# Optimization experiments

Measured on AMD Instinct MI355X. Metric: run time of the kernel, lower is better.

Reference implementation:

```python
import jax, jax.numpy as jnp
import numpy as np

H, C = 4, 32          # GAT heads, per-head dim
NH = 4                # transformer heads


def layer_norm(x, g, b, eps=1e-5):
    mu = x.mean(-1, keepdims=True)
    var = ((x - mu) ** 2).mean(-1, keepdims=True)
    return (x - mu) / jnp.sqrt(var + eps) * g + b


def setup_inputs() -> dict:
    key = jax.random.key(0)
    ks = jax.random.split(key, 16)
    B, T, N, F = 256, 72, 5, 10
    D, FF = 128, 256
    # full directed graph on 5 stations, no self loops (E=20)
    ei = np.array([[i, j] for i in range(N) for j in range(N) if i != j], dtype=np.int32).T
    s = 0.1
    return {
        'x': jax.random.normal(ks[0], (B, T, N, F), jnp.float32),
        'edge_index': jnp.asarray(ei),
        'gcn_w': jax.random.normal(ks[1], (F, 64), jnp.float32) * s,
        'gcn_b': jnp.zeros((64,), jnp.float32),
        'gat_w': jax.random.normal(ks[2], (64, H * C), jnp.float32) * s,
        'gat_a_src': jax.random.normal(ks[3], (H, C), jnp.float32) * s,
        'gat_a_dst': jax.random.normal(ks[4], (H, C), jnp.float32) * s,
        'gat_b': jnp.zeros((H * C,), jnp.float32),
        'gln_g': jnp.ones((D,), jnp.float32),
        'gln_b': jnp.zeros((D,), jnp.float32),
        'tw_qkv': jax.random.normal(ks[5], (3, D, 3 * D), jnp.float32) * s,
        'tb_qkv': jnp.zeros((3, 3 * D), jnp.float32),
        'tw_o': jax.random.normal(ks[6], (3, D, D), jnp.float32) * s,
        'tb_o': jnp.zeros((3, D), jnp.float32),
        'ln1_g': jnp.ones((3, D), jnp.float32),
        'ln1_b': jnp.zeros((3, D), jnp.float32),
        'w_ff1': jax.random.normal(ks[7], (3, D, FF), jnp.float32) * s,
        'b_ff1': jnp.zeros((3, FF), jnp.float32),
        'w_ff2': jax.random.normal(ks[8], (3, FF, D), jnp.float32) * s,
        'b_ff2': jnp.zeros((3, D), jnp.float32),
        'ln2_g': jnp.ones((3, D), jnp.float32),
        'ln2_b': jnp.zeros((3, D), jnp.float32),
        'hw1': jax.random.normal(ks[9], (6, D, D // 2), jnp.float32) * s,
        'hb1': jnp.zeros((6, D // 2), jnp.float32),
        'hw2': jax.random.normal(ks[10], (6, D // 2, 5), jnp.float32) * s,
        'hb2': jnp.zeros((6, 5), jnp.float32),
    }


def reference(x, edge_index, gcn_w, gcn_b, gat_w, gat_a_src, gat_a_dst, gat_b,
              gln_g, gln_b, tw_qkv, tb_qkv, tw_o, tb_o, ln1_g, ln1_b,
              w_ff1, b_ff1, w_ff2, b_ff2, ln2_g, ln2_b, hw1, hb1, hw2, hb2):
    B, T, N, F = x.shape
    D = gln_g.shape[0]

    # ---- frozen GCN encoder (torch.no_grad): symmetric-normalized A with self loops
    src, dst = edge_index[0], edge_index[1]
    loop = jnp.arange(N, dtype=src.dtype)
    src2 = jnp.concatenate([src, loop])
    dst2 = jnp.concatenate([dst, loop])
    A = jnp.zeros((N, N), x.dtype).at[dst2, src2].add(1.0)
    deg = A.sum(1)
    dinv = jnp.where(deg > 0, deg ** -0.5, 0.0)
    Anorm = dinv[:, None] * A * dinv[None, :]
    xw = jnp.einsum('btnf,fh->btnh', x, gcn_w) + gcn_b
    gcn = jnp.tanh(jnp.einsum('ij,btjh->btih', Anorm, xw))
    gcn = jax.lax.stop_gradient(gcn)  # encoder is frozen + no_grad

    # ---- GATConv over batched graph (self loops added, PyG default), eval mode (no dropout)
    h = jnp.einsum('btnf,fhc->btnhc', gcn, gat_w.reshape(gcn.shape[-1], H, C))
    a_s = (h * gat_a_src).sum(-1)                         # [B,T,N,H]
    a_d = (h * gat_a_dst).sum(-1)
    e = a_s[:, :, src2, :] + a_d[:, :, dst2, :]           # [B,T,E2,H]
    e = jnp.where(e > 0, e, 0.2 * e)                      # LeakyReLU(0.2)
    eT = jnp.moveaxis(e, 2, 0)                            # [E2,B,T,H]
    m = jax.ops.segment_max(eT, dst2, num_segments=N)
    ex = jnp.exp(eT - m[dst2])
    denom = jax.ops.segment_sum(ex, dst2, num_segments=N)
    alpha = ex / denom[dst2]                              # scatter-softmax per dst node
    hsrc = jnp.moveaxis(h, 2, 0)[src2]                    # [E2,B,T,H,C]
    agg = jax.ops.segment_sum(alpha[..., None] * hsrc, dst2, num_segments=N)
    gat = jnp.moveaxis(agg, 0, 2).reshape(B, T, N, H * C) + gat_b
    gat = layer_norm(gat, gln_g, gln_b)

    # ---- mean-pool stations, positional encoding
    z = gat.mean(2)                                       # [B,T,D]
    pos = jnp.arange(T, dtype=jnp.float32)[:, None]
    div = jnp.exp(jnp.arange(0, D, 2, dtype=jnp.float32) * (-np.log(10000.0) / D))
    pe = jnp.zeros((T, D), x.dtype).at[:, 0::2].set(jnp.sin(pos * div)).at[:, 1::2].set(jnp.cos(pos * div))
    z = z + pe

    # ---- post-norm transformer encoder (relu FF), eval mode
    dh = D // NH
    scale = jnp.sqrt(jnp.asarray(dh, x.dtype))
    for i in range(tw_qkv.shape[0]):
        qkv = z @ tw_qkv[i] + tb_qkv[i]
        q, k, v = jnp.split(qkv, 3, axis=-1)
        q = q.reshape(B, T, NH, dh)
        k = k.reshape(B, T, NH, dh)
        v = v.reshape(B, T, NH, dh)
        att = jax.nn.softmax(jnp.einsum('bqhd,bkhd->bhqk', q, k) / scale, axis=-1)
        o = jnp.einsum('bhqk,bkhd->bqhd', att, v).reshape(B, T, D)
        z = layer_norm(z + o @ tw_o[i] + tb_o[i], ln1_g[i], ln1_b[i])
        ff = jax.nn.relu(z @ w_ff1[i] + b_ff1[i]) @ w_ff2[i] + b_ff2[i]
        z = layer_norm(z + ff, ln2_g[i], ln2_b[i])

    # ---- multi-horizon forecast heads on last timestep -> stacked [6,B,5]
    last = z[:, -1]
    h1 = jax.nn.relu(jnp.einsum('bd,kdm->kbm', last, hw1) + hb1[:, None, :])
    out = jnp.einsum('kbm,kms->kbs', h1, hw2) + hb2[:, None, :]
    return out
```

## Files before the change

### kernel.cpp

```cpp
#include <hip/hip_runtime.h>
#include <hip/hip_bf16.h>

#define B_  256
#define T_  72
#define N_  5
#define F_  10
#define D_  128
#define HH_ 4
#define CC_ 32
#define FF_ 256
#define BT_ (B_*T_)
#define E2MAX 32

#define WS_Z    256
#define WS_QKV  (WS_Z + BT_*D_)
#define WS_OBUF (WS_QKV + BT_*3*D_)
#define WS_WBF  (WS_OBUF + BT_*D_)

#define WOFF_QKV(i)  ((i)*49152)
#define WOFF_O(i)    (147456 + (i)*16384)
#define WOFF_FF1(i)  (196608 + (i)*32768)
#define WOFF_FF2(i)  (294912 + (i)*32768)
#define WOFF_GATW    393216

#define MZF_OFF   0
#define MSB_OFF   38016
#define MSQ_OFF   70784
#define MSK_OFF   92544
#define MVT_OFF   114304
#define MOB_OFF   140928
#define MSMEM_BYTES 162688

typedef __attribute__((ext_vector_type(8))) short bf16x8;
typedef __attribute__((ext_vector_type(4))) float f32x4;

__device__ __forceinline__ unsigned short bf16_rne(float x) {
    unsigned u = __float_as_uint(x);
    unsigned r = (u + 0x7FFFu + ((u >> 16) & 1u)) >> 16;
    return (unsigned short)r;
}
__device__ __forceinline__ unsigned bf16pk(float a, float b) {
    return (unsigned)bf16_rne(a) | ((unsigned)bf16_rne(b) << 16);
}
__device__ __forceinline__ float bf2f(short s) {
    return __uint_as_float(((unsigned)(unsigned short)s) << 16);
}
__device__ __forceinline__ bf16x8 cvt8(const float* p) {
    float4 a = *(const float4*)p;
    float4 b = *(const float4*)(p + 4);
    unsigned u[4] = {bf16pk(a.x, a.y), bf16pk(a.z, a.w), bf16pk(b.x, b.y), bf16pk(b.z, b.w)};
    return *(bf16x8*)u;
}

__global__ void setup_kernel(const int* __restrict__ ei, float* __restrict__ ws, int E) {
    if (threadIdx.x != 0 || blockIdx.x != 0) return;
    int* wsi = (int*)ws;
    const int N = N_;
    int E2 = E + N;
    int src2[E2MAX], dst2[E2MAX];
    for (int e = 0; e < E; ++e) { src2[e] = ei[e]; dst2[e] = ei[E + e]; }
    for (int n = 0; n < N; ++n) { src2[E + n] = n; dst2[E + n] = n; }
    float A[N_ * N_];
    for (int i = 0; i < N * N; ++i) A[i] = 0.f;
    for (int e = 0; e < E2; ++e) A[dst2[e] * N + src2[e]] += 1.f;
    float dinv[N_];
    for (int n = 0; n < N; ++n) {
        float s = 0.f;
        for (int j = 0; j < N; ++j) s += A[n * N + j];
        dinv[n] = (s > 0.f) ? rsqrtf(s) : 0.f;
    }
    for (int n = 0; n < N; ++n)
        for (int j = 0; j < N; ++j)
            ws[n * N + j] = dinv[n] * A[n * N + j] * dinv[j];
    int cnt[N_];
    for (int n = 0; n < N; ++n) cnt[n] = 0;
    for (int e = 0; e < E2; ++e) cnt[dst2[e]]++;
    int off = 0;
    for (int n = 0; n < N; ++n) { wsi[96 + n] = off; off += cnt[n]; }
    wsi[96 + N] = off;
    int cur[N_];
    for (int n = 0; n < N; ++n) cur[n] = wsi[96 + n];
    for (int e = 0; e < E2; ++e) wsi[104 + cur[dst2[e]]++] = e;
    for (int e = 0; e < E2; ++e) { wsi[32 + e] = src2[e]; wsi[64 + e] = dst2[e]; }
}

__global__ __launch_bounds__(256) void prep_kernel(
    const float* __restrict__ tw_qkv, const float* __restrict__ tw_o,
    const float* __restrict__ w_ff1, const float* __restrict__ w_ff2,
    const float* __restrict__ gat_w, short* __restrict__ wbf)
{
    __shared__ float s_t[64][65];
    const int tid = threadIdx.x;
    int t = blockIdx.x;
    const float* src; short* dst; int R, C, tr, tc;
    if (t >= 96) { int q = t - 96; src = gat_w; dst = wbf + WOFF_GATW; R = 64; C = 128; tr = 0; tc = q; }
    else {
        int layer = t / 32, r32 = t % 32;
        if (r32 < 12)      { src = tw_qkv + layer * (128*384); dst = wbf + WOFF_QKV(layer); R = 128; C = 384; tr = r32 / 6;  tc = r32 % 6; }
        else if (r32 < 16) { int q = r32 - 12; src = tw_o + layer * 16384; dst = wbf + WOFF_O(layer);  R = 128; C = 128; tr = q >> 1; tc = q & 1; }
        else if (r32 < 24) { int q = r32 - 16; src = w_ff1 + layer * 32768; dst = wbf + WOFF_FF1(layer); R = 128; C = 256; tr = q >> 2; tc = q & 3; }
        else               { int q = r32 - 24; src = w_ff2 + layer * 32768; dst = wbf + WOFF_FF2(layer); R = 256; C = 128; tr = q >> 1; tc = q & 1; }
    }
    #pragma unroll
    for (int it = 0; it < 16; ++it) {
        int e = it * 256 + tid;
        int r = e >> 6, c = e & 63;
        s_t[r][c] = src[(size_t)(tr*64 + r) * C + tc*64 + c];
    }
    __syncthreads();
    #pragma unroll
    for (int it = 0; it < 16; ++it) {
        int e = it * 256 + tid;
        int c = e >> 6, r = e & 63;
        dst[(size_t)(tc*64 + c) * R + tr*64 + r] = (short)bf16_rne(s_t[r][c]);
    }
}

__device__ __forceinline__ bf16x8 ld_frag(const short* s, int row, int kbase, int ldk) {
    return *(const bf16x8*)&s[row * ldk + (kbase ^ ((row & 7) << 3))];
}
__device__ __forceinline__ void stage_b(short* s_b, const short* __restrict__ src, int tid) {
    const uint4* s4 = (const uint4*)src;
    #pragma unroll
    for (int it = 0; it < 8; ++it) {
        int c = it * 256 + tid;
        int row = c >> 4, ke = (c & 15) * 8;
        *(uint4*)&s_b[row * 128 + (ke ^ ((row & 7) << 3))] = s4[c];
    }
}

__global__ __launch_bounds__(256) void gcn_h_mfma(
    const float* __restrict__ x, const float* __restrict__ gcn_w, const float* __restrict__ gcn_b,
    const float* __restrict__ a_src, const float* __restrict__ a_dst,
    const float* __restrict__ ws, const short* __restrict__ gwT,
    short* __restrict__ hbuf, float* __restrict__ asb, float* __restrict__ adb)
{
    __shared__ float s_x[16 * 50];
    __shared__ float s_an[25];
    __shared__ short s_gcn[80 * 64];

    const int tid = threadIdx.x;
    const int tok0 = blockIdx.x * 16;

    for (int i = tid; i < 16 * 50; i += 256) s_x[i] = x[(size_t)tok0 * 50 + i];
    if (tid < 25) s_an[tid] = ws[tid];
    __syncthreads();

    #pragma unroll
    for (int it = 0; it < 2; ++it) {
        int idx = it * 256 + tid;
        int tl = idx >> 5, kp = idx & 31;
        int k0 = kp * 2;
        float w0[F_], w1[F_];
        #pragma unroll
        for (int f = 0; f < F_; ++f) { w0[f] = gcn_w[f * 64 + k0]; w1[f] = gcn_w[f * 64 + k0 + 1]; }
        float b0 = gcn_b[k0], b1 = gcn_b[k0 + 1];
        float xw0[N_], xw1[N_];
        #pragma unroll
        for (int n = 0; n < N_; ++n) {
            float a0 = b0, a1 = b1;
            #pragma unroll
            for (int f = 0; f < F_; ++f) {
                float xv = s_x[tl * 50 + n * 10 + f];
                a0 += xv * w0[f]; a1 += xv * w1[f];
            }
            xw0[n] = a0; xw1[n] = a1;
        }
        #pragma unroll
        for (int n = 0; n < N_; ++n) {
            float s0 = 0.f, s1 = 0.f;
            #pragma unroll
            for (int j = 0; j < N_; ++j) { float an = s_an[n * 5 + j]; s0 += an * xw0[j]; s1 += an * xw1[j]; }
            float e0 = __expf(2.f * fabsf(s0)), e1 = __expf(2.f * fabsf(s1));
            float t0 = copysignf(1.f - 2.f / (e0 + 1.f), s0);
            float t1 = copysignf(1.f - 2.f / (e1 + 1.f), s1);
            int row = tl * 5 + n;
            *(unsigned*)&s_gcn[row * 64 + (k0 ^ ((row & 7) << 3))] = bf16pk(t0, t1);
        }
    }
    __syncthreads();

    const int w = tid >> 6, lane = tid & 63;
    const int c = lane & 15, g = lane >> 4;
    const int kf = g * 8;
    bf16x8 bfr[2][2];
    #pragma unroll
    for (int nn = 0; nn < 2; ++nn)
        #pragma unroll
        for (int k0 = 0; k0 < 2; ++k0)
            bfr[nn][k0] = *(const bf16x8*)&gwT[(w * 32 + nn * 16 + c) * 64 + k0 * 32 + kf];
    const float as0 = a_src[w * 32 + c],      as1 = a_src[w * 32 + 16 + c];
    const float ad0 = a_dst[w * 32 + c],      ad1 = a_dst[w * 32 + 16 + c];
    #pragma unroll
    for (int m = 0; m < 5; ++m) {
        bf16x8 af0 = ld_frag(s_gcn, m * 16 + c, kf, 64);
        bf16x8 af1 = ld_frag(s_gcn, m * 16 + c, 32 + kf, 64);
        f32x4 a0 = {0,0,0,0}, a1 = {0,0,0,0};
        a0 = __builtin_amdgcn_mfma_f32_16x16x32_bf16(af0, bfr[0][0], a0, 0, 0, 0);
        a0 = __builtin_amdgcn_mfma_f32_16x16x32_bf16(af1, bfr[0][1], a0, 0, 0, 0);
        a1 = __builtin_amdgcn_mfma_f32_16x16x32_bf16(af0, bfr[1][0], a1, 0, 0, 0);
        a1 = __builtin_amdgcn_mfma_f32_16x16x32_bf16(af1, bfr[1][1], a1, 0, 0, 0);
        float ps[4], pd[4];
        #pragma unroll
        for (int i = 0; i < 4; ++i) {
            int row = m * 16 + g * 4 + i;
            size_t gr = (size_t)(tok0 * 5 + row) * 128;
            hbuf[gr + w * 32 + c]      = (short)bf16_rne(a0[i]);
            hbuf[gr + w * 32 + 16 + c] = (short)bf16_rne(a1[i]);
            ps[i] = a0[i] * as0 + a1[i] * as1;
            pd[i] = a0[i] * ad0 + a1[i] * ad1;
        }
        #pragma unroll
        for (int mm = 1; mm < 16; mm <<= 1)
            #pragma unroll
            for (int i = 0; i < 4; ++i) { ps[i] += __shfl_xor(ps[i], mm); pd[i] += __shfl_xor(pd[i], mm); }
        if (c == 0) {
            #pragma unroll
            for (int i = 0; i < 4; ++i) {
                int row = m * 16 + g * 4 + i;
                asb[(size_t)(tok0 * 5 + row) * 4 + w] = ps[i];
                adb[(size_t)(tok0 * 5 + row) * 4 + w] = pd[i];
            }
        }
    }
}

__global__ __launch_bounds__(256) void gat_agg(
    const short* __restrict__ hbuf, const float* __restrict__ asb, const float* __restrict__ adb,
    const float* __restrict__ gat_b, const float* __restrict__ gln_g, const float* __restrict__ gln_b,
    const float* __restrict__ ws, float* __restrict__ z, int E2)
{
    __shared__ int   s_src[E2MAX], s_csr_off[N_ + 1], s_csr_e[E2MAX];
    __shared__ float s_alpha[4][E2MAX][4];
    __shared__ short s_h[4 * 5 * 128];

    const int tid = threadIdx.x;
    const int wv = tid >> 6, lane = tid & 63;
    const int tok = blockIdx.x * 4 + wv;
    const int* wsi = (const int*)ws;

    if (tid < E2) { s_src[tid] = wsi[32 + tid]; s_csr_e[tid] = wsi[104 + tid]; }
    if (tid < N_ + 1) s_csr_off[tid] = wsi[96 + tid];
    {
        const uint4* hb4 = (const uint4*)(hbuf + (size_t)blockIdx.x * 4 * 5 * 128);
        uint4* sh4 = (uint4*)s_h;
        #pragma unroll
        for (int it = 0; it < 2; ++it) {
            int i = it * 256 + tid;
            if (i < 320) sh4[i] = hb4[i];
        }
    }
    __syncthreads();

    if (lane < 20) {
        int dn = lane >> 2, head = lane & 3;
        int j0 = s_csr_off[dn], j1 = s_csr_off[dn + 1];
        float adv = adb[(size_t)(tok * 5 + dn) * 4 + head];
        float mx = -1e30f;
        for (int j = j0; j < j1; ++j) {
            int e = s_csr_e[j];
            float ev = asb[(size_t)(tok * 5 + s_src[e]) * 4 + head] + adv;
            ev = ev > 0.f ? ev : 0.2f * ev;
            mx = fmaxf(mx, ev);
        }
        float den = 0.f;
        for (int j = j0; j < j1; ++j) {
            int e = s_csr_e[j];
            float ev = asb[(size_t)(tok * 5 + s_src[e]) * 4 + head] + adv;
            ev = ev > 0.f ? ev : 0.2f * ev;
            float ex = __expf(ev - mx);
            den += ex;
            s_alpha[wv][e][head] = ex;
        }
        float r = 1.f / den;
        for (int j = j0; j < j1; ++j) s_alpha[wv][s_csr_e[j]][head] *= r;
    }
    __syncthreads();

    const int h0 = lane >> 5, h1 = 2 + (lane >> 5);
    const float gb0 = gat_b[lane],      gb1 = gat_b[lane + 64];
    const float gg0 = gln_g[lane],      gg1 = gln_g[lane + 64];
    const float gB0 = gln_b[lane],      gB1 = gln_b[lane + 64];
    float v0[N_], v1[N_];
    #pragma unroll
    for (int n = 0; n < N_; ++n) {
        float a0 = 0.f, a1 = 0.f;
        int j0 = s_csr_off[n], j1 = s_csr_off[n + 1];
        for (int j = j0; j < j1; ++j) {
            int e = s_csr_e[j];
            int rb = (wv * 5 + s_src[e]) * 128;
            a0 += s_alpha[wv][e][h0] * bf2f(s_h[rb + lane]);
            a1 += s_alpha[wv][e][h1] * bf2f(s_h[rb + lane + 64]);
        }
        v0[n] = a0 + gb0; v1[n] = a1 + gb1;
    }
    float r1[N_], r2[N_];
    #pragma unroll
    for (int n = 0; n < N_; ++n) { r1[n] = v0[n] + v1[n]; r2[n] = v0[n]*v0[n] + v1[n]*v1[n]; }
    #pragma unroll
    for (int mm = 1; mm < 64; mm <<= 1)
        #pragma unroll
        for (int n = 0; n < N_; ++n) { r1[n] += __shfl_xor(r1[n], mm); r2[n] += __shfl_xor(r2[n], mm); }
    float z0 = 0.f, z1 = 0.f;
    #pragma unroll
    for (int n = 0; n < N_; ++n) {
        float mu = r1[n] * (1.f / D_);
        float var = r2[n] * (1.f / D_) - mu * mu;
        float rstd = rsqrtf(var + 1e-5f);
        z0 += (v0[n] - mu) * rstd * gg0 + gB0;
        z1 += (v1[n] - mu) * rstd * gg1 + gB1;
    }
    z0 *= (1.f / N_); z1 *= (1.f / N_);
    const float cpe = -9.210340371976184f / (float)D_;
    int t = tok % T_;
    float dv0 = __expf((float)(lane & ~1) * cpe);
    float dv1 = __expf((float)((lane + 64) & ~1) * cpe);
    float ang0 = (float)t * dv0, ang1 = (float)t * dv1;
    z0 += (lane & 1) ? __cosf(ang0) : __sinf(ang0);
    z1 += (lane & 1) ? __cosf(ang1) : __sinf(ang1);
    z[(size_t)tok * D_ + lane] = z0;
    z[(size_t)tok * D_ + 64 + lane] = z1;
}

__global__ __launch_bounds__(256, 1) void layers_fused(
    const float* __restrict__ zg, const short* __restrict__ wbf,
    const float* __restrict__ tb_qkv, const float* __restrict__ tb_o,
    const float* __restrict__ ln1_g, const float* __restrict__ ln1_b,
    const float* __restrict__ b_ff1, const float* __restrict__ b_ff2,
    const float* __restrict__ ln2_g, const float* __restrict__ ln2_b,
    const float* __restrict__ hw1, const float* __restrict__ hb1,
    const float* __restrict__ hw2, const float* __restrict__ hb2,
    float* __restrict__ out)
{
    extern __shared__ char smem[];
    float* s_zf = (float*)(smem + MZF_OFF);
    short* s_b  = (short*)(smem + MSB_OFF);
    short* s_q  = (short*)(smem + MSQ_OFF);
    short* s_k  = (short*)(smem + MSK_OFF);
    short* s_vt = (short*)(smem + MVT_OFF);
    short* s_ob = (short*)(smem + MOB_OFF);
    short* s_f  = s_q;
    short* s_z1 = s_vt;

    const int tid = threadIdx.x;
    const int w = tid >> 6, lane = tid & 63;
    const int c = lane & 15, g = lane >> 4;
    const int kf = g * 8;
    const int b = blockIdx.x;

    for (int idx = tid; idx < 72 * 128; idx += 256) {
        int r = idx >> 7, col = idx & 127;
        s_zf[r * 132 + col] = zg[(size_t)(b * T_ + r) * D_ + col];
    }
    for (int idx = tid; idx < 128 * 32; idx += 256) {
        int ch = idx >> 5, key = 72 + (idx & 31);
        s_vt[ch * 104 + key] = 0;
    }
    __syncthreads();

    for (int L = 0; L < 3; ++L) {
        const short* Wq = wbf + WOFF_QKV(L);
        const short* Wo = wbf + WOFF_O(L);
        const short* W1 = wbf + WOFF_FF1(L);
        const short* W2 = wbf + WOFF_FF2(L);
        const float* bq = tb_qkv + L * 384;
        const float* bo = tb_o + L * D_;
        const float* g1 = ln1_g + L * D_, *be1 = ln1_b + L * D_;
        const float* b1 = b_ff1 + L * FF_, *b2 = b_ff2 + L * D_;
        const float* g2 = ln2_g + L * D_, *be2 = ln2_b + L * D_;

        for (int ch = 0; ch < 3; ++ch) {
            __syncthreads();
            stage_b(s_b, Wq + ch * 16384, tid);
            __syncthreads();
            bf16x8 Bf[2][4];
            float bvj[2];
            #pragma unroll
            for (int j = 0; j < 2; ++j) {
                int n0 = w * 2 + j;
                int brow = n0 * 16 + c;
                #pragma unroll
                for (int k0 = 0; k0 < 4; ++k0) Bf[j][k0] = ld_frag(s_b, brow, k0 * 32 + kf, 128);
                bvj[j] = bq[ch * 128 + n0 * 16 + c];
            }
            #pragma unroll
            for (int m = 0; m < 5; ++m) {
                int arow = m * 16 + c;
                bool valid = arow < 72;
                bf16x8 Af[4];
                bf16x8 z8 = {0,0,0,0,0,0,0,0};
                #pragma unroll
                for (int k0 = 0; k0 < 4; ++k0)
                    Af[k0] = valid ? cvt8(&s_zf[arow * 132 + k0 * 32 + kf]) : z8;
                #pragma unroll
                for (int j = 0; j < 2; ++j) {
                    int n0 = w * 2 + j;
                    f32x4 acc = {bvj[j], bvj[j], bvj[j], bvj[j]};
                    #pragma unroll
                    for (int k0 = 0; k0 < 4; ++k0)
                        acc = __builtin_amdgcn_mfma_f32_16x16x32_bf16(Af[k0], Bf[j][k0], acc, 0, 0, 0);
                    int wcol = n0 * 16 + c;
                    #pragma unroll
                    for (int i = 0; i < 4; ++i) {
                        int lrow = m * 16 + g * 4 + i;
                        short v = (short)bf16_rne(acc[i]);
                        if (ch == 0)      s_q[lrow * 136 + wcol] = v;
                        else if (ch == 1) s_k[lrow * 136 + wcol] = v;
                        else              s_vt[wcol * 104 + lrow] = v;
                    }
                }
            }
        }
        __syncthreads();

        {
            short* pstrip = s_b + w * 16 * 104;
            for (int t2 = lane; t2 < 16 * 16; t2 += 64) {
                int r = t2 >> 4, col = 80 + (t2 & 15);
                pstrip[r * 104 + col] = 0;
            }
            const float scale = 0.17677669529663687f;
            #pragma unroll
            for (int m = 0; m < 5; ++m) {
                bf16x8 aq = *(const bf16x8*)&s_q[(m * 16 + c) * 136 + w * 32 + kf];
                float ps[5][4], mx[4], den[4];
                #pragma unroll
                for (int i = 0; i < 4; ++i) mx[i] = -1e30f;
                #pragma unroll
                for (int n0 = 0; n0 < 5; ++n0) {
                    bf16x8 bk = *(const bf16x8*)&s_k[(n0 * 16 + c) * 136 + w * 32 + kf];
                    f32x4 z4 = {0,0,0,0};
                    f32x4 accS = __builtin_amdgcn_mfma_f32_16x16x32_bf16(aq, bk, z4, 0, 0, 0);
                    #pragma unroll
                    for (int i = 0; i < 4; ++i) {
                        float s = accS[i] * scale;
                        if (n0 == 4 && c >= 8) s = -1e30f;
                        ps[n0][i] = s;
                        mx[i] = fmaxf(mx[i], s);
                    }
                }
                #pragma unroll
                for (int mm = 1; mm < 16; mm <<= 1)
                    #pragma unroll
                    for (int i = 0; i < 4; ++i) mx[i] = fmaxf(mx[i], __shfl_xor(mx[i], mm));
                #pragma unroll
                for (int i = 0; i < 4; ++i) den[i] = 0.f;
                #pragma unroll
                for (int n0 = 0; n0 < 5; ++n0)
                    #pragma unroll
                    for (int i = 0; i < 4; ++i) { float e = __expf(ps[n0][i] - mx[i]); ps[n0][i] = e; den[i] += e; }
                #pragma unroll
                for (int mm = 1; mm < 16; mm <<= 1)
                    #pragma unroll
                    for (int i = 0; i < 4; ++i) den[i] += __shfl_xor(den[i], mm);
                float rden[4];
                #pragma unroll
                for (int i = 0; i < 4; ++i) rden[i] = 1.f / den[i];
                #pragma unroll
                for (int n0 = 0; n0 < 5; ++n0)
                    #pragma unroll
                    for (int i = 0; i < 4; ++i)
                        pstrip[(g * 4 + i) * 104 + n0 * 16 + c] = (short)bf16_rne(ps[n0][i] * rden[i]);
                f32x4 accO[2] = {{0,0,0,0},{0,0,0,0}};
                #pragma unroll
                for (int kt = 0; kt < 3; ++kt) {
                    bf16x8 ap = *(const bf16x8*)&pstrip[c * 104 + kt * 32 + kf];
                    #pragma unroll
                    for (int n0 = 0; n0 < 2; ++n0) {
                        bf16x8 bv = *(const bf16x8*)&s_vt[(w * 32 + n0 * 16 + c) * 104 + kt * 32 + kf];
                        accO[n0] = __builtin_amdgcn_mfma_f32_16x16x32_bf16(ap, bv, accO[n0], 0, 0, 0);
                    }
                }
                #pragma unroll
                for (int n0 = 0; n0 < 2; ++n0)
                    #pragma unroll
                    for (int i = 0; i < 4; ++i)
                        s_ob[(m * 16 + g * 4 + i) * 136 + w * 32 + n0 * 16 + c] = (short)bf16_rne(accO[n0][i]);
            }
        }
        __syncthreads();

        stage_b(s_b, Wo, tid);
        __syncthreads();
        for (int m = w; m < 5; m += 4) {
            bf16x8 Af[4];
            #pragma unroll
            for (int k0 = 0; k0 < 4; ++k0)
                Af[k0] = *(const bf16x8*)&s_ob[(m * 16 + c) * 136 + k0 * 32 + kf];
            f32x4 acc[8];
            #pragma unroll
            for (int n0 = 0; n0 < 8; ++n0) {
                float bv = bo[n0 * 16 + c];
                acc[n0] = (f32x4){bv, bv, bv, bv};
                int brow = n0 * 16 + c;
                #pragma unroll
                for (int k0 = 0; k0 < 4; ++k0) {
                    bf16x8 bfg = ld_frag(s_b, brow, k0 * 32 + kf, 128);
                    acc[n0] = __builtin_amdgcn_mfma_f32_16x16x32_bf16(Af[k0], bfg, acc[n0], 0, 0, 0);
                }
            }
            #pragma unroll
            for (int n0 = 0; n0 < 8; ++n0)
                #pragma unroll
                for (int i = 0; i < 4; ++i) {
                    int row = m * 16 + g * 4 + i;
                    acc[n0][i] += (row < 72) ? s_zf[row * 132 + n0 * 16 + c] : 0.f;
                }
            float s1[4] = {0,0,0,0}, s2[4] = {0,0,0,0};
            #pragma unroll
            for (int n0 = 0; n0 < 8; ++n0)
                #pragma unroll
                for (int i = 0; i < 4; ++i) { float v = acc[n0][i]; s1[i] += v; s2[i] += v * v; }
            #pragma unroll
            for (int mm = 1; mm < 16; mm <<= 1)
                #pragma unroll
                for (int i = 0; i < 4; ++i) { s1[i] += __shfl_xor(s1[i], mm); s2[i] += __shfl_xor(s2[i], mm); }
            #pragma unroll
            for (int i = 0; i < 4; ++i) {
                float mu = s1[i] * (1.f / D_);
                float var = s2[i] * (1.f / D_) - mu * mu;
                float rstd = rsqrtf(var + 1e-5f);
                int row = m * 16 + g * 4 + i;
                #pragma unroll
                for (int n0 = 0; n0 < 8; ++n0) {
                    float v = (acc[n0][i] - mu) * rstd * g1[n0 * 16 + c] + be1[n0 * 16 + c];
                    if (row < 72) s_zf[row * 132 + n0 * 16 + c] = v;
                    s_z1[row * 136 + n0 * 16 + c] = (short)bf16_rne(v);
                }
            }
        }

        for (int ch = 0; ch < 2; ++ch) {
            __syncthreads();
            stage_b(s_b, W1 + ch * 16384, tid);
            __syncthreads();
            bf16x8 Bf[2][4];
            float bvj[2];
            #pragma unroll
            for (int j = 0; j < 2; ++j) {
                int n0 = w * 2 + j;
                int brow = n0 * 16 + c;
                #pragma unroll
                for (int k0 = 0; k0 < 4; ++k0) Bf[j][k0] = ld_frag(s_b, brow, k0 * 32 + kf, 128);
                bvj[j] = b1[ch * 128 + n0 * 16 + c];
            }
            #pragma unroll
            for (int m = 0; m < 5; ++m) {
                bf16x8 Af[4];
                #pragma unroll
                for (int k0 = 0; k0 < 4; ++k0)
                    Af[k0] = *(const bf16x8*)&s_z1[(m * 16 + c) * 136 + k0 * 32 + kf];
                #pragma unroll
                for (int j = 0; j < 2; ++j) {
                    int n0 = w * 2 + j;
                    f32x4 acc = {bvj[j], bvj[j], bvj[j], bvj[j]};
                    #pragma unroll
                    for (int k0 = 0; k0 < 4; ++k0)
                        acc = __builtin_amdgcn_mfma_f32_16x16x32_bf16(Af[k0], Bf[j][k0], acc, 0, 0, 0);
                    #pragma unroll
                    for (int i = 0; i < 4; ++i) {
                        int lrow = m * 16 + g * 4 + i;
                        s_f[lrow * 264 + ch * 128 + n0 * 16 + c] = (short)bf16_rne(fmaxf(acc[i], 0.f));
                    }
                }
            }
        }

        f32x4 accA[8], accB[8];
        #pragma unroll
        for (int n0 = 0; n0 < 8; ++n0) {
            float bv = b2[n0 * 16 + c];
            accA[n0] = (f32x4){bv, bv, bv, bv};
            accB[n0] = (f32x4){bv, bv, bv, bv};
        }
        for (int kc = 0; kc < 2; ++kc) {
            __syncthreads();
            {
                #pragma unroll
                for (int it = 0; it < 8; ++it) {
                    int cc = it * 256 + tid;
                    int row = cc >> 4, ke = (cc & 15) * 8;
                    uint4 v = *(const uint4*)&W2[row * 256 + kc * 128 + ke];
                    *(uint4*)&s_b[row * 128 + (ke ^ ((row & 7) << 3))] = v;
                }
            }
            __syncthreads();
            {
                bf16x8 Af[4];
                #pragma unroll
                for (int k0 = 0; k0 < 4; ++k0)
                    Af[k0] = *(const bf16x8*)&s_f[(w * 16 + c) * 264 + kc * 128 + k0 * 32 + kf];
                #pragma unroll
                for (int n0 = 0; n0 < 8; ++n0) {
                    int brow = n0 * 16 + c;
                    #pragma unroll
                    for (int k0 = 0; k0 < 4; ++k0) {
                        bf16x8 bfg = ld_frag(s_b, brow, k0 * 32 + kf, 128);
                        accA[n0] = __builtin_amdgcn_mfma_f32_16x16x32_bf16(Af[k0], bfg, accA[n0], 0, 0, 0);
                    }
                }
            }
            if (w == 0) {
                bf16x8 Af[4];
                #pragma unroll
                for (int k0 = 0; k0 < 4; ++k0)
                    Af[k0] = *(const bf16x8*)&s_f[(64 + c) * 264 + kc * 128 + k0 * 32 + kf];
                #pragma unroll
                for (int n0 = 0; n0 < 8; ++n0) {
                    int brow = n0 * 16 + c;
                    #pragma unroll
                    for (int k0 = 0; k0 < 4; ++k0) {
                        bf16x8 bfg = ld_frag(s_b, brow, k0 * 32 + kf, 128);
                        accB[n0] = __builtin_amdgcn_mfma_f32_16x16x32_bf16(Af[k0], bfg, accB[n0], 0, 0, 0);
                    }
                }
            }
        }
        {
            #pragma unroll
            for (int n0 = 0; n0 < 8; ++n0)
                #pragma unroll
                for (int i = 0; i < 4; ++i) {
                    int row = w * 16 + g * 4 + i;
                    accA[n0][i] += (row < 72) ? s_zf[row * 132 + n0 * 16 + c] : 0.f;
                }
            float s1[4] = {0,0,0,0}, s2[4] = {0,0,0,0};
            #pragma unroll
            for (int n0 = 0; n0 < 8; ++n0)
                #pragma unroll
                for (int i = 0; i < 4; ++i) { float v = accA[n0][i]; s1[i] += v; s2[i] += v * v; }
            #pragma unroll
            for (int mm = 1; mm < 16; mm <<= 1)
                #pragma unroll
                for (int i = 0; i < 4; ++i) { s1[i] += __shfl_xor(s1[i], mm); s2[i] += __shfl_xor(s2[i], mm); }
            #pragma unroll
            for (int i = 0; i < 4; ++i) {
                float mu = s1[i] * (1.f / D_);
                float var = s2[i] * (1.f / D_) - mu * mu;
                float rstd = rsqrtf(var + 1e-5f);
                int row = w * 16 + g * 4 + i;
                if (row < 72)
                    #pragma unroll
                    for (int n0 = 0; n0 < 8; ++n0)
                        s_zf[row * 132 + n0 * 16 + c] =
                            (accA[n0][i] - mu) * rstd * g2[n0 * 16 + c] + be2[n0 * 16 + c];
            }
        }
        if (w == 0) {
            #pragma unroll
            for (int n0 = 0; n0 < 8; ++n0)
                #pragma unroll
                for (int i = 0; i < 4; ++i) {
                    int row = 64 + g * 4 + i;
                    accB[n0][i] += (row < 72) ? s_zf[row * 132 + n0 * 16 + c] : 0.f;
                }
            float s1[4] = {0,0,0,0}, s2[4] = {0,0,0,0};
            #pragma unroll
            for (int n0 = 0; n0 < 8; ++n0)
                #pragma unroll
                for (int i = 0; i < 4; ++i) { float v = accB[n0][i]; s1[i] += v; s2[i] += v * v; }
            #pragma unroll
            for (int mm = 1; mm < 16; mm <<= 1)
                #pragma unroll
                for (int i = 0; i < 4; ++i) { s1[i] += __shfl_xor(s1[i], mm); s2[i] += __shfl_xor(s2[i], mm); }
            #pragma unroll
            for (int i = 0; i < 4; ++i) {
                float mu = s1[i] * (1.f / D_);
                float var = s2[i] * (1.f / D_) - mu * mu;
                float rstd = rsqrtf(var + 1e-5f);
                int row = 64 + g * 4 + i;
                if (row < 72)
                    #pragma unroll
                    for (int n0 = 0; n0 < 8; ++n0)
                        s_zf[row * 132 + n0 * 16 + c] =
                            (accB[n0][i] - mu) * rstd * g2[n0 * 16 + c] + be2[n0 * 16 + c];
            }
        }
    }

    __syncthreads();
    float* s_h1 = (float*)s_b;
    for (int t2 = tid; t2 < 384; t2 += 256) {
        int k = t2 >> 6, j = t2 & 63;
        float acc = hb1[k * 64 + j];
        const float* w1p = hw1 + (size_t)k * D_ * 64 + j;
        for (int d = 0; d < D_; ++d) acc += s_zf[71 * 132 + d] * w1p[d * 64];
        s_h1[k * 64 + j] = fmaxf(acc, 0.f);
    }
    __syncthreads();
    if (tid < 30) {
        int k = tid / 5, s = tid % 5;
        float o = hb2[k * 5 + s];
        const float* w2p = hw2 + (size_t)k * 64 * 5 + s;
        for (int j = 0; j < 64; ++j) o += s_h1[k * 64 + j] * w2p[j * 5];
        out[(size_t)k * (B_ * 5) + b * 5 + s] = o;
    }
}

extern "C" void kernel_launch(void* const* d_in, const int* in_sizes, int n_in,
                              void* d_out, int out_size, void* d_ws, size_t ws_size,
                              hipStream_t stream) {
    const float* x      = (const float*)d_in[0];
    const int*   ei     = (const int*)  d_in[1];
    const float* gcn_w  = (const float*)d_in[2];
    const float* gcn_b  = (const float*)d_in[3];
    const float* gat_w  = (const float*)d_in[4];
    const float* a_src  = (const float*)d_in[5];
    const float* a_dst  = (const float*)d_in[6];
    const float* gat_b  = (const float*)d_in[7];
    const float* gln_g  = (const float*)d_in[8];
    const float* gln_b  = (const float*)d_in[9];
    const float* tw_qkv = (const float*)d_in[10];
    const float* tb_qkv = (const float*)d_in[11];
    const float* tw_o   = (const float*)d_in[12];
    const float* tb_o   = (const float*)d_in[13];
    const float* ln1_g  = (const float*)d_in[14];
    const float* ln1_b  = (const float*)d_in[15];
    const float* w_ff1  = (const float*)d_in[16];
    const float* b_ff1  = (const float*)d_in[17];
    const float* w_ff2  = (const float*)d_in[18];
    const float* b_ff2  = (const float*)d_in[19];
    const float* ln2_g  = (const float*)d_in[20];
    const float* ln2_b  = (const float*)d_in[21];
    const float* hw1    = (const float*)d_in[22];
    const float* hb1    = (const float*)d_in[23];
    const float* hw2    = (const float*)d_in[24];
    const float* hb2    = (const float*)d_in[25];
    float* out = (float*)d_out;
    float* ws  = (float*)d_ws;

    float* z   = ws + WS_Z;
    short* wbf = (short*)(ws + WS_WBF);

    short* hbuf = (short*)(ws + WS_QKV);
    float* asb  = ws + WS_OBUF;
    float* adb  = ws + WS_OBUF + BT_ * 5 * 4;

    const int E = in_sizes[1] / 2;
    const int E2 = E + N_;

    static bool attr_set = false;
    if (!attr_set) {
        hipFuncSetAttribute((const void*)layers_fused,
                            hipFuncAttributeMaxDynamicSharedMemorySize, MSMEM_BYTES);
        attr_set = true;
    }

    setup_kernel<<<1, 64, 0, stream>>>(ei, ws, E);
    prep_kernel<<<98, 256, 0, stream>>>(tw_qkv, tw_o, w_ff1, w_ff2, gat_w, wbf);
    gcn_h_mfma<<<BT_ / 16, 256, 0, stream>>>(x, gcn_w, gcn_b, a_src, a_dst, ws,
                                             wbf + WOFF_GATW, hbuf, asb, adb);
    gat_agg<<<BT_ / 4, 256, 0, stream>>>(hbuf, asb, adb, gat_b, gln_g, gln_b, ws, z, E2);
    layers_fused<<<B_, 256, MSMEM_BYTES, stream>>>(z, wbf, tb_qkv, tb_o,
                                                   ln1_g, ln1_b, b_ff1, b_ff2,
                                                   ln2_g, ln2_b, hw1, hb1, hw2, hb2, out);
}
```

Measured before the change: 355.6 us.

## Double layers_fused block to eight wavefronts and redistribute per-wave GEMM and attention work

The fused transformer kernel now launches 512 threads (8 waves) per batch element instead of 256. Each wave computes one 16-column tile in the QKV and FF1 GEMMs. Attention is split by head and by query-row range across the waves, and the Wo/FF2 row tiles use five waves, which removes the serialized extra tile that wave 0 used to handle. The aim is more parallelism and latency hiding per CU, since the grid is only 256 blocks. The cost is extra idle waves in some phases and higher register pressure under the 512-thread launch bound.

Measured after the change: 289.7 us. 18.5% less time.

```diff
diff --git a/kernel.cpp b/kernel.cpp
--- a/kernel.cpp
+++ b/kernel.cpp
@@ -128,6 +128,15 @@
         *(uint4*)&s_b[row * 128 + (ke ^ ((row & 7) << 3))] = s4[c];
     }
 }
+__device__ __forceinline__ void stage_b512(short* s_b, const short* __restrict__ src, int tid) {
+    const uint4* s4 = (const uint4*)src;
+    #pragma unroll
+    for (int it = 0; it < 4; ++it) {
+        int c = it * 512 + tid;
+        int row = c >> 4, ke = (c & 15) * 8;
+        *(uint4*)&s_b[row * 128 + (ke ^ ((row & 7) << 3))] = s4[c];
+    }
+}
 
 __global__ __launch_bounds__(256) void gcn_h_mfma(
     const float* __restrict__ x, const float* __restrict__ gcn_w, const float* __restrict__ gcn_b,
@@ -322,7 +331,7 @@
     z[(size_t)tok * D_ + 64 + lane] = z1;
 }
 
-__global__ __launch_bounds__(256, 1) void layers_fused(
+__global__ __launch_bounds__(512, 1) void layers_fused(
     const float* __restrict__ zg, const short* __restrict__ wbf,
     const float* __restrict__ tb_qkv, const float* __restrict__ tb_o,
     const float* __restrict__ ln1_g, const float* __restrict__ ln1_b,
@@ -348,11 +357,11 @@
     const int kf = g * 8;
     const int b = blockIdx.x;
 
-    for (int idx = tid; idx < 72 * 128; idx += 256) {
+    for (int idx = tid; idx < 72 * 128; idx += 512) {
         int r = idx >> 7, col = idx & 127;
         s_zf[r * 132 + col] = zg[(size_t)(b * T_ + r) * D_ + col];
     }
-    for (int idx = tid; idx < 128 * 32; idx += 256) {
+    for (int idx = tid; idx < 128 * 32; idx += 512) {
         int ch = idx >> 5, key = 72 + (idx & 31);
         s_vt[ch * 104 + key] = 0;
     }
@@ -371,18 +380,15 @@
 
         for (int ch = 0; ch < 3; ++ch) {
             __syncthreads();
-            stage_b(s_b, Wq + ch * 16384, tid);
+            stage_b512(s_b, Wq + ch * 16384, tid);
             __syncthreads();
-            bf16x8 Bf[2][4];
-            float bvj[2];
-            #pragma unroll
-            for (int j = 0; j < 2; ++j) {
-                int n0 = w * 2 + j;
-                int brow = n0 * 16 + c;
-                #pragma unroll
-                for (int k0 = 0; k0 < 4; ++k0) Bf[j][k0] = ld_frag(s_b, brow, k0 * 32 + kf, 128);
-                bvj[j] = bq[ch * 128 + n0 * 16 + c];
-            }
+            const int n0 = w;
+            const int brow = n0 * 16 + c;
+            bf16x8 Bf[4];
+            #pragma unroll
+            for (int k0 = 0; k0 < 4; ++k0) Bf[k0] = ld_frag(s_b, brow, k0 * 32 + kf, 128);
+            const float bv = bq[ch * 128 + n0 * 16 + c];
+            const int wcol = n0 * 16 + c;
             #pragma unroll
             for (int m = 0; m < 5; ++m) {
                 int arow = m * 16 + c;
@@ -392,43 +398,40 @@
                 #pragma unroll
                 for (int k0 = 0; k0 < 4; ++k0)
                     Af[k0] = valid ? cvt8(&s_zf[arow * 132 + k0 * 32 + kf]) : z8;
-                #pragma unroll
-                for (int j = 0; j < 2; ++j) {
-                    int n0 = w * 2 + j;
-                    f32x4 acc = {bvj[j], bvj[j], bvj[j], bvj[j]};
-                    #pragma unroll
-                    for (int k0 = 0; k0 < 4; ++k0)
-                        acc = __builtin_amdgcn_mfma_f32_16x16x32_bf16(Af[k0], Bf[j][k0], acc, 0, 0, 0);
-                    int wcol = n0 * 16 + c;
-                    #pragma unroll
-                    for (int i = 0; i < 4; ++i) {
-                        int lrow = m * 16 + g * 4 + i;
-                        short v = (short)bf16_rne(acc[i]);
-                        if (ch == 0)      s_q[lrow * 136 + wcol] = v;
-                        else if (ch == 1) s_k[lrow * 136 + wcol] = v;
-                        else              s_vt[wcol * 104 + lrow] = v;
-                    }
+                f32x4 acc = {bv, bv, bv, bv};
+                #pragma unroll
+                for (int k0 = 0; k0 < 4; ++k0)
+                    acc = __builtin_amdgcn_mfma_f32_16x16x32_bf16(Af[k0], Bf[k0], acc, 0, 0, 0);
+                #pragma unroll
+                for (int i = 0; i < 4; ++i) {
+                    int lrow = m * 16 + g * 4 + i;
+                    short v = (short)bf16_rne(acc[i]);
+                    if (ch == 0)      s_q[lrow * 136 + wcol] = v;
+                    else if (ch == 1) s_k[lrow * 136 + wcol] = v;
+                    else              s_vt[wcol * 104 + lrow] = v;
                 }
             }
         }
         __syncthreads();
 
         {
-            short* pstrip = s_b + w * 16 * 104;
-            for (int t2 = lane; t2 < 16 * 16; t2 += 64) {
-                int r = t2 >> 4, col = 80 + (t2 & 15);
+            short* pstrip = s_b + w * (16 * 104);
+            for (int t2 = lane; t2 < 16 * 24; t2 += 64) {
+                int r = t2 / 24, col = 80 + (t2 % 24);
                 pstrip[r * 104 + col] = 0;
             }
+            const int h = w & 3;
+            const int mlo = (w >> 2) ? 3 : 0;
+            const int mhi = (w >> 2) ? 5 : 3;
             const float scale = 0.17677669529663687f;
-            #pragma unroll
-            for (int m = 0; m < 5; ++m) {
-                bf16x8 aq = *(const bf16x8*)&s_q[(m * 16 + c) * 136 + w * 32 + kf];
+            for (int m = mlo; m < mhi; ++m) {
+                bf16x8 aq = *(const bf16x8*)&s_q[(m * 16 + c) * 136 + h * 32 + kf];
                 float ps[5][4], mx[4], den[4];
                 #pragma unroll
                 for (int i = 0; i < 4; ++i) mx[i] = -1e30f;
                 #pragma unroll
                 for (int n0 = 0; n0 < 5; ++n0) {
-                    bf16x8 bk = *(const bf16x8*)&s_k[(n0 * 16 + c) * 136 + w * 32 + kf];
+                    bf16x8 bk = *(const bf16x8*)&s_k[(n0 * 16 + c) * 136 + h * 32 + kf];
                     f32x4 z4 = {0,0,0,0};
                     f32x4 accS = __builtin_amdgcn_mfma_f32_16x16x32_bf16(aq, bk, z4, 0, 0, 0);
                     #pragma unroll
@@ -467,7 +470,7 @@
                     bf16x8 ap = *(const bf16x8*)&pstrip[c * 104 + kt * 32 + kf];
                     #pragma unroll
                     for (int n0 = 0; n0 < 2; ++n0) {
-                        bf16x8 bv = *(const bf16x8*)&s_vt[(w * 32 + n0 * 16 + c) * 104 + kt * 32 + kf];
+                        bf16x8 bv = *(const bf16x8*)&s_vt[(h * 32 + n0 * 16 + c) * 104 + kt * 32 + kf];
                         accO[n0] = __builtin_amdgcn_mfma_f32_16x16x32_bf16(ap, bv, accO[n0], 0, 0, 0);
                     }
                 }
@@ -475,14 +478,15 @@
                 for (int n0 = 0; n0 < 2; ++n0)
                     #pragma unroll
                     for (int i = 0; i < 4; ++i)
-                        s_ob[(m * 16 + g * 4 + i) * 136 + w * 32 + n0 * 16 + c] = (short)bf16_rne(accO[n0][i]);
+                        s_ob[(m * 16 + g * 4 + i) * 136 + h * 32 + n0 * 16 + c] = (short)bf16_rne(accO[n0][i]);
             }
         }
         __syncthreads();
 
-        stage_b(s_b, Wo, tid);
+        stage_b512(s_b, Wo, tid);
         __syncthreads();
-        for (int m = w; m < 5; m += 4) {
+        if (w < 5) {
+            const int m = w;
             bf16x8 Af[4];
             #pragma unroll
             for (int k0 = 0; k0 < 4; ++k0)
@@ -532,60 +536,51 @@
 
         for (int ch = 0; ch < 2; ++ch) {
             __syncthreads();
-            stage_b(s_b, W1 + ch * 16384, tid);
+            stage_b512(s_b, W1 + ch * 16384, tid);
             __syncthreads();
-            bf16x8 Bf[2][4];
-            float bvj[2];
-            #pragma unroll
-            for (int j = 0; j < 2; ++j) {
-                int n0 = w * 2 + j;
-                int brow = n0 * 16 + c;
-                #pragma unroll
-                for (int k0 = 0; k0 < 4; ++k0) Bf[j][k0] = ld_frag(s_b, brow, k0 * 32 + kf, 128);
-                bvj[j] = b1[ch * 128 + n0 * 16 + c];
-            }
+            const int n0 = w;
+            const int brow = n0 * 16 + c;
+            bf16x8 Bf[4];
+            #pragma unroll
+            for (int k0 = 0; k0 < 4; ++k0) Bf[k0] = ld_frag(s_b, brow, k0 * 32 + kf, 128);
+            const float bv = b1[ch * 128 + n0 * 16 + c];
             #pragma unroll
             for (int m = 0; m < 5; ++m) {
                 bf16x8 Af[4];
                 #pragma unroll
                 for (int k0 = 0; k0 < 4; ++k0)
                     Af[k0] = *(const bf16x8*)&s_z1[(m * 16 + c) * 136 + k0 * 32 + kf];
-                #pragma unroll
-                for (int j = 0; j < 2; ++j) {
-                    int n0 = w * 2 + j;
-                    f32x4 acc = {bvj[j], bvj[j], bvj[j], bvj[j]};
-                    #pragma unroll
-                    for (int k0 = 0; k0 < 4; ++k0)
-                        acc = __builtin_amdgcn_mfma_f32_16x16x32_bf16(Af[k0], Bf[j][k0], acc, 0, 0, 0);
-                    #pragma unroll
-                    for (int i = 0; i < 4; ++i) {
-                        int lrow = m * 16 + g * 4 + i;
-                        s_f[lrow * 264 + ch * 128 + n0 * 16 + c] = (short)bf16_rne(fmaxf(acc[i], 0.f));
-                    }
-                }
-            }
-        }
-
-        f32x4 accA[8], accB[8];
+                f32x4 acc = {bv, bv, bv, bv};
+                #pragma unroll
+                for (int k0 = 0; k0 < 4; ++k0)
+                    acc = __builtin_amdgcn_mfma_f32_16x16x32_bf16(Af[k0], Bf[k0], acc, 0, 0, 0);
+                #pragma unroll
+                for (int i = 0; i < 4; ++i) {
+                    int lrow = m * 16 + g * 4 + i;
+                    s_f[lrow * 264 + ch * 128 + n0 * 16 + c] = (short)bf16_rne(fmaxf(acc[i], 0.f));
+                }
+            }
+        }
+
+        f32x4 acc2[8];
         #pragma unroll
         for (int n0 = 0; n0 < 8; ++n0) {
             float bv = b2[n0 * 16 + c];
-            accA[n0] = (f32x4){bv, bv, bv, bv};
-            accB[n0] = (f32x4){bv, bv, bv, bv};
+            acc2[n0] = (f32x4){bv, bv, bv, bv};
         }
         for (int kc = 0; kc < 2; ++kc) {
             __syncthreads();
             {
                 #pragma unroll
-                for (int it = 0; it < 8; ++it) {
-                    int cc = it * 256 + tid;
+                for (int it = 0; it < 4; ++it) {
+                    int cc = it * 512 + tid;
                     int row = cc >> 4, ke = (cc & 15) * 8;
                     uint4 v = *(const uint4*)&W2[row * 256 + kc * 128 + ke];
                     *(uint4*)&s_b[row * 128 + (ke ^ ((row & 7) << 3))] = v;
                 }
             }
             __syncthreads();
-            {
+            if (w < 5) {
                 bf16x8 Af[4];
                 #pragma unroll
                 for (int k0 = 0; k0 < 4; ++k0)
@@ -596,39 +591,25 @@
                     #pragma unroll
                     for (int k0 = 0; k0 < 4; ++k0) {
                         bf16x8 bfg = ld_frag(s_b, brow, k0 * 32 + kf, 128);
-                        accA[n0] = __builtin_amdgcn_mfma_f32_16x16x32_bf16(Af[k0], bfg, accA[n0], 0, 0, 0);
+                        acc2[n0] = __builtin_amdgcn_mfma_f32_16x16x32_bf16(Af[k0], bfg, acc2[n0], 0, 0, 0);
                     }
                 }
             }
-            if (w == 0) {
-                bf16x8 Af[4];
-                #pragma unroll
-                for (int k0 = 0; k0 < 4; ++k0)
-                    Af[k0] = *(const bf16x8*)&s_f[(64 + c) * 264 + kc * 128 + k0 * 32 + kf];
-                #pragma unroll
-                for (int n0 = 0; n0 < 8; ++n0) {
-                    int brow = n0 * 16 + c;
-                    #pragma unroll
-                    for (int k0 = 0; k0 < 4; ++k0) {
-                        bf16x8 bfg = ld_frag(s_b, brow, k0 * 32 + kf, 128);
-                        accB[n0] = __builtin_amdgcn_mfma_f32_16x16x32_bf16(Af[k0], bfg, accB[n0], 0, 0, 0);
-                    }
-                }
-            }
-        }
-        {
+        }
+        if (w < 5) {
+            const int m = w;
             #pragma unroll
             for (int n0 = 0; n0 < 8; ++n0)
                 #pragma unroll
                 for (int i = 0; i < 4; ++i) {
-                    int row = w * 16 + g * 4 + i;
-                    accA[n0][i] += (row < 72) ? s_zf[row * 132 + n0 * 16 + c] : 0.f;
+                    int row = m * 16 + g * 4 + i;
+                    acc2[n0][i] += (row < 72) ? s_zf[row * 132 + n0 * 16 + c] : 0.f;
                 }
             float s1[4] = {0,0,0,0}, s2[4] = {0,0,0,0};
             #pragma unroll
             for (int n0 = 0; n0 < 8; ++n0)
                 #pragma unroll
-                for (int i = 0; i < 4; ++i) { float v = accA[n0][i]; s1[i] += v; s2[i] += v * v; }
+                for (int i = 0; i < 4; ++i) { float v = acc2[n0][i]; s1[i] += v; s2[i] += v * v; }
             #pragma unroll
             for (int mm = 1; mm < 16; mm <<= 1)
                 #pragma unroll
@@ -638,49 +619,19 @@
                 float mu = s1[i] * (1.f / D_);
                 float var = s2[i] * (1.f / D_) - mu * mu;
                 float rstd = rsqrtf(var + 1e-5f);
-                int row = w * 16 + g * 4 + i;
+                int row = m * 16 + g * 4 + i;
                 if (row < 72)
                     #pragma unroll
                     for (int n0 = 0; n0 < 8; ++n0)
                         s_zf[row * 132 + n0 * 16 + c] =
-                            (accA[n0][i] - mu) * rstd * g2[n0 * 16 + c] + be2[n0 * 16 + c];
-            }
-        }
-        if (w == 0) {
-            #pragma unroll
-            for (int n0 = 0; n0 < 8; ++n0)
-                #pragma unroll
-                for (int i = 0; i < 4; ++i) {
-                    int row = 64 + g * 4 + i;
-                    accB[n0][i] += (row < 72) ? s_zf[row * 132 + n0 * 16 + c] : 0.f;
-                }
-            float s1[4] = {0,0,0,0}, s2[4] = {0,0,0,0};
-            #pragma unroll
-            for (int n0 = 0; n0 < 8; ++n0)
-                #pragma unroll
-                for (int i = 0; i < 4; ++i) { float v = accB[n0][i]; s1[i] += v; s2[i] += v * v; }
-            #pragma unroll
-            for (int mm = 1; mm < 16; mm <<= 1)
-                #pragma unroll
-                for (int i = 0; i < 4; ++i) { s1[i] += __shfl_xor(s1[i], mm); s2[i] += __shfl_xor(s2[i], mm); }
-            #pragma unroll
-            for (int i = 0; i < 4; ++i) {
-                float mu = s1[i] * (1.f / D_);
-                float var = s2[i] * (1.f / D_) - mu * mu;
-                float rstd = rsqrtf(var + 1e-5f);
-                int row = 64 + g * 4 + i;
-                if (row < 72)
-                    #pragma unroll
-                    for (int n0 = 0; n0 < 8; ++n0)
-                        s_zf[row * 132 + n0 * 16 + c] =
-                            (accB[n0][i] - mu) * rstd * g2[n0 * 16 + c] + be2[n0 * 16 + c];
+                            (acc2[n0][i] - mu) * rstd * g2[n0 * 16 + c] + be2[n0 * 16 + c];
             }
         }
     }
 
     __syncthreads();
     float* s_h1 = (float*)s_b;
-    for (int t2 = tid; t2 < 384; t2 += 256) {
+    for (int t2 = tid; t2 < 384; t2 += 512) {
         int k = t2 >> 6, j = t2 & 63;
         float acc = hb1[k * 64 + j];
         const float* w1p = hw1 + (size_t)k * D_ * 64 + j;
@@ -751,7 +702,7 @@
     gcn_h_mfma<<<BT_ / 16, 256, 0, stream>>>(x, gcn_w, gcn_b, a_src, a_dst, ws,
                                              wbf + WOFF_GATW, hbuf, asb, adb);
     gat_agg<<<BT_ / 4, 256, 0, stream>>>(hbuf, asb, adb, gat_b, gln_g, gln_b, ws, z, E2);
-    layers_fused<<<B_, 256, MSMEM_BYTES, stream>>>(z, wbf, tb_qkv, tb_o,
+    layers_fused<<<B_, 512, MSMEM_BYTES, stream>>>(z, wbf, tb_qkv, tb_o,
                                                    ln1_g, ln1_b, b_ff1, b_ff2,
                                                    ln2_g, ln2_b, hw1, hb1, hw2, hb2, out);
 }
```
